# Kernel optimization log

Hardware: AMD Instinct MI355X
Metric: run time of the kernel (lower is better)

The kernel has to match this reference:

```python
import jax, jax.numpy as jnp
import numpy as np

B, S, N, M = 64, 512, 512, 128   # batch, sensory_size, state_size, motor_size
UNFOLDS = 6
DT = 0.1  # elapsed_time


def _gate(v, mu, sigma):
    # piecewise-linear 'sigmoid': clip((v - mu + sigma) / (2 sigma), 0, 1)
    # v: [B, P] -> [B, P, 1] broadcast against [P, N]
    return jnp.clip((v[..., None] - mu + sigma) / (2.0 * sigma), 0.0, 1.0)


def setup_inputs() -> dict:
    key = jax.random.key(0)
    ks = jax.random.split(key, 12)
    u = lambda k, sh, lo, hi: jax.random.uniform(k, sh, jnp.float32, lo, hi)
    inputs = jax.random.normal(ks[0], (B, S), dtype=jnp.float32)
    states = jax.random.normal(ks[1], (B, N), dtype=jnp.float32) * 0.1
    # parameters per _init_ranges
    tau = u(ks[2], (N,), 0.001, 2.0)
    b = u(ks[3], (N,), -0.2, 0.2)
    erev = jnp.where(jax.random.bernoulli(ks[4], 0.8, (N, N)), 1.0, -1.0).astype(jnp.float32)
    w = u(ks[5], (N, N), 0.001, 1.0)
    sigma = jnp.full((N, N), 0.5, jnp.float32)
    mu = jnp.full((N, N), 0.5, jnp.float32)
    sensory_erev = jnp.where(jax.random.bernoulli(ks[6], 0.8, (S, N)), 1.0, -1.0).astype(jnp.float32)
    sensory_w = u(ks[7], (S, N), 0.001, 1.0)
    sensory_sigma = jnp.full((S, N), 0.5, jnp.float32)
    sensory_mu = jnp.full((S, N), 0.5, jnp.float32)
    sparsity_mask = jax.random.bernoulli(ks[8], 0.3, (N, N)).astype(jnp.float32)
    sensory_sparsity_mask = jax.random.bernoulli(ks[9], 0.3, (S, N)).astype(jnp.float32)
    input_w = jnp.ones((S,), jnp.float32)
    input_b = jnp.zeros((S,), jnp.float32)
    output_w = jnp.ones((M,), jnp.float32)
    output_b = jnp.zeros((M,), jnp.float32)
    return dict(inputs=inputs, states=states, tau=tau, b=b, erev=erev, w=w,
                sigma=sigma, mu=mu, sensory_erev=sensory_erev, sensory_w=sensory_w,
                sensory_sigma=sensory_sigma, sensory_mu=sensory_mu,
                sparsity_mask=sparsity_mask, sensory_sparsity_mask=sensory_sparsity_mask,
                input_w=input_w, input_b=input_b, output_w=output_w, output_b=output_b)


def reference(inputs, states, tau, b, erev, w, sigma, mu,
              sensory_erev, sensory_w, sensory_sigma, sensory_mu,
              sparsity_mask, sensory_sparsity_mask,
              input_w, input_b, output_w, output_b):
    # input mapping (affine)
    x = inputs * input_w + input_b                                   # [B, S]
    # sensory synapses, computed once
    sa = _gate(x, sensory_mu, sensory_sigma) * sensory_sparsity_mask  # [B, S, N]
    s_rev = jnp.einsum('bsn,sn->bn', sa, sensory_erev)               # [B, N]
    s_w = jnp.einsum('bsn,sn->bn', sa, sensory_w)                    # [B, N]
    delta = DT / UNFOLDS

    def step(v, _):
        g = _gate(v, mu, sigma) * sparsity_mask                      # [B, N, N]
        sum_rev = jnp.einsum('bij,ij->bj', g, erev) + s_rev + b      # sum over presynaptic i
        sum_w = jnp.einsum('bij,ij->bj', g, w) + s_w
        k = 1.0 / (1.0 + sum_w)
        taun = tau * k
        q = taun / (taun + delta)
        v_new = q * v + (1.0 - q) * k * sum_rev
        return v_new, None

    v, _ = jax.lax.scan(step, states, None, length=UNFOLDS)
    # output mapping: slice last M neurons (M < N), then affine
    out = v[:, -M:] * output_w + output_b                            # [B, M]
    return out, v
```

## Files before the change

### kernel.cpp

```cpp
#include <hip/hip_runtime.h>
#include <string.h>

constexpr int cB = 64, cS = 512, cN = 512, cM = 128, cUNF = 6;
constexpr float cDELTA = 0.016666666666666666f;

constexpr int KB = 4;
constexpr int JT = 32;
constexpr int NJT = cN / JT;
constexpr int IC = 32;
constexpr int ILEN = cN / IC;
constexpr int NT = JT * IC;
constexpr int NB = (cB / KB) * NJT;

constexpr size_t OFF_EW  = 0;
constexpr size_t OFF_VA  = (size_t)cN * cN * 2;
constexpr size_t OFF_VB  = OFF_VA + (size_t)cB * cN;
constexpr size_t OFF_CTR = OFF_VB + (size_t)cB * cN;
constexpr int CTR_INTS = 512 + 16;

__device__ __forceinline__ float clamp01(float x) {
    return __builtin_amdgcn_fmed3f(x, 0.0f, 1.0f);
}

__global__ __launch_bounds__(NT)
void k_sns(const float* __restrict__ inputs, const float* __restrict__ states,
           const float* __restrict__ tau,    const float* __restrict__ bias,
           const float* __restrict__ erev,   const float* __restrict__ wgt,
           const float* __restrict__ sigma,  const float* __restrict__ mu,
           const float* __restrict__ serev,  const float* __restrict__ swgt,
           const float* __restrict__ ssigma, const float* __restrict__ smu,
           const float* __restrict__ mask,   const float* __restrict__ smask,
           const float* __restrict__ inw,    const float* __restrict__ inb,
           const float* __restrict__ outw,   const float* __restrict__ outb,
           float* __restrict__ out, float* __restrict__ ws)
{
    float2* EW = (float2*)(ws + OFF_EW);
    float* vA  = ws + OFF_VA;
    float* vB  = ws + OFF_VB;
    int*   ctr = (int*)(ws + OFF_CTR);

    const int tid = threadIdx.x, bid = blockIdx.x;
    const int jt = (bid & 7) * 2 + ((bid >> 3) & 1);
    const int bg = bid >> 4;
    const int b0 = bg * KB, j0 = jt * JT;
    const int jl = tid & (JT - 1), ic = tid >> 5;
    const int j = j0 + jl;
    int* barU  = ctr + bg * 16;
    int* barI  = ctr + 256 + jt * 16;
    int* flagp = ctr + 512 + jt;

    __shared__ float stage[cN * KB];
    __shared__ float redR[KB * IC * JT];
    __shared__ float redW[KB * IC * JT];
    __shared__ int   s_fast;

    {
        int i   = bg * 32 + ic;
        int idx = i * cN + j;
        float mk = mask[idx];
        float2 ew = make_float2(erev[idx] * mk, wgt[idx] * mk);
        unsigned long long bits;
        memcpy(&bits, &ew, 8);
        __hip_atomic_store((unsigned long long*)&EW[idx], bits,
                           __ATOMIC_RELAXED, __HIP_MEMORY_SCOPE_AGENT);
        if (!((sigma[idx] == 0.5f) && (mu[idx] == 0.5f)))
            __hip_atomic_fetch_or(flagp, 1, __ATOMIC_RELAXED, __HIP_MEMORY_SCOPE_AGENT);
    }

#pragma unroll
    for (int r = 0; r < (cS * KB) / NT; ++r) {
        int t = tid + r * NT;
        int bb = t & 3, s = t >> 2;
        stage[t] = fmaf(inputs[(b0 + bb) * cS + s], inw[s], inb[s]);
    }
    __syncthreads();
    {
        float aR[KB] = {0.f, 0.f, 0.f, 0.f}, aW[KB] = {0.f, 0.f, 0.f, 0.f};
        int idx = (ic * ILEN) * cN + j;
        int xo  = (ic * ILEN) * KB;
#pragma unroll 4
        for (int ii = 0; ii < ILEN; ++ii, idx += cN, xo += KB) {
            float sg = ssigma[idx];
            float a  = 0.5f / sg;
            float c  = fmaf(-smu[idx], a, 0.5f);
            float mk = smask[idx];
            float e  = serev[idx] * mk;
            float wv = swgt[idx] * mk;
            const float4 xv = *(const float4*)&stage[xo];
            float g;
            g = clamp01(fmaf(xv.x, a, c)); aR[0] = fmaf(g, e, aR[0]); aW[0] = fmaf(g, wv, aW[0]);
            g = clamp01(fmaf(xv.y, a, c)); aR[1] = fmaf(g, e, aR[1]); aW[1] = fmaf(g, wv, aW[1]);
            g = clamp01(fmaf(xv.z, a, c)); aR[2] = fmaf(g, e, aR[2]); aW[2] = fmaf(g, wv, aW[2]);
            g = clamp01(fmaf(xv.w, a, c)); aR[3] = fmaf(g, e, aR[3]); aW[3] = fmaf(g, wv, aW[3]);
        }
#pragma unroll
        for (int b = 0; b < KB; ++b) {
            redR[(b * IC + ic) * JT + jl] = aR[b];
            redW[(b * IC + ic) * JT + jl] = aW[b];
        }
    }
    __syncthreads();

    float my_srb = 0.f, my_sw = 0.f, my_tau = 0.f, my_ow = 0.f, my_ob = 0.f;
    int my_gidx = 0, my_mi = -1;
    if (tid < JT * KB) {
        int jj = tid & (JT - 1), bb = tid >> 5;
        float r = 0.f, wv = 0.f;
#pragma unroll
        for (int c2 = 0; c2 < IC; ++c2) {
            r  += redR[(bb * IC + c2) * JT + jj];
            wv += redW[(bb * IC + c2) * JT + jj];
        }
        int jg  = j0 + jj;
        my_gidx = (b0 + bb) * cN + jg;
        my_srb  = r + bias[jg];
        my_sw   = wv;
        my_tau  = tau[jg];
        if (jg >= cN - cM) {
            int m = jg - (cN - cM);
            my_ow = outw[m]; my_ob = outb[m];
            my_mi = (b0 + bb) * cM + m;
        }
    }

    __syncthreads();
    if (tid == 0) {
        __hip_atomic_fetch_add(barI, 1, __ATOMIC_RELAXED, __HIP_MEMORY_SCOPE_AGENT);
        while (__hip_atomic_load(barI, __ATOMIC_RELAXED, __HIP_MEMORY_SCOPE_AGENT) < NJT)
            __builtin_amdgcn_s_sleep(1);
        s_fast = (0 == __hip_atomic_load(flagp, __ATOMIC_RELAXED, __HIP_MEMORY_SCOPE_AGENT));
    }
    __syncthreads();
    const int fast = s_fast;

    const float* vin = states;
    for (int u = 0; u < cUNF; ++u) {
        float* vout = (u == cUNF - 1) ? (out + cB * cM) : ((u & 1) ? vA : vB);

#pragma unroll
        for (int r = 0; r < (cN * KB) / NT; ++r) {
            int t = tid + r * NT;
            int bb = t & 3, ii = t >> 2;
            float vv = __hip_atomic_load(&vin[(b0 + bb) * cN + ii],
                                         __ATOMIC_RELAXED, __HIP_MEMORY_SCOPE_AGENT);
            stage[t] = fast ? clamp01(vv) : vv;
        }
        __syncthreads();

        float vold = 0.f;
        if (tid < JT * KB)
            vold = __hip_atomic_load(&vin[my_gidx],
                                     __ATOMIC_RELAXED, __HIP_MEMORY_SCOPE_AGENT);

        float aR[KB] = {0.f, 0.f, 0.f, 0.f}, aW[KB] = {0.f, 0.f, 0.f, 0.f};
        if (fast) {
            int idx = (ic * ILEN) * cN + j;
            int vo  = (ic * ILEN) * KB;
#pragma unroll 8
            for (int ii = 0; ii < ILEN; ++ii, idx += cN, vo += KB) {
                const float2 ew = EW[idx];
                const float4 g4 = *(const float4*)&stage[vo];
                aR[0] = fmaf(g4.x, ew.x, aR[0]); aW[0] = fmaf(g4.x, ew.y, aW[0]);
                aR[1] = fmaf(g4.y, ew.x, aR[1]); aW[1] = fmaf(g4.y, ew.y, aW[1]);
                aR[2] = fmaf(g4.z, ew.x, aR[2]); aW[2] = fmaf(g4.z, ew.y, aW[2]);
                aR[3] = fmaf(g4.w, ew.x, aR[3]); aW[3] = fmaf(g4.w, ew.y, aW[3]);
            }
        } else {
            int idx = (ic * ILEN) * cN + j;
            int vo  = (ic * ILEN) * KB;
#pragma unroll 4
            for (int ii = 0; ii < ILEN; ++ii, idx += cN, vo += KB) {
                float sg = sigma[idx];
                float a  = 0.5f / sg;
                float c  = fmaf(-mu[idx], a, 0.5f);
                float2 ew = EW[idx];
                const float4 vv = *(const float4*)&stage[vo];
                float g;
                g = clamp01(fmaf(vv.x, a, c)); aR[0] = fmaf(g, ew.x, aR[0]); aW[0] = fmaf(g, ew.y, aW[0]);
                g = clamp01(fmaf(vv.y, a, c)); aR[1] = fmaf(g, ew.x, aR[1]); aW[1] = fmaf(g, ew.y, aW[1]);
                g = clamp01(fmaf(vv.z, a, c)); aR[2] = fmaf(g, ew.x, aR[2]); aW[2] = fmaf(g, ew.y, aW[2]);
                g = clamp01(fmaf(vv.w, a, c)); aR[3] = fmaf(g, ew.x, aR[3]); aW[3] = fmaf(g, ew.y, aW[3]);
            }
        }
#pragma unroll
        for (int b = 0; b < KB; ++b) {
            redR[(b * IC + ic) * JT + jl] = aR[b];
            redW[(b * IC + ic) * JT + jl] = aW[b];
        }
        __syncthreads();

        if (tid < JT * KB) {
            int jj = tid & (JT - 1), bb = tid >> 5;
            float r = 0.f, wv = 0.f;
#pragma unroll
            for (int c2 = 0; c2 < IC; ++c2) {
                r  += redR[(bb * IC + c2) * JT + jj];
                wv += redW[(bb * IC + c2) * JT + jj];
            }
            r  += my_srb;
            wv += my_sw;
            float k    = 1.0f / (1.0f + wv);
            float taun = my_tau * k;
            float inv  = 1.0f / (taun + cDELTA);
            float vn   = (taun * inv) * vold + (cDELTA * inv) * k * r;
            if (u == cUNF - 1) {
                vout[my_gidx] = vn;
                if (my_mi >= 0) out[my_mi] = fmaf(vn, my_ow, my_ob);
            } else {
                __hip_atomic_store(&vout[my_gidx], vn,
                                   __ATOMIC_RELAXED, __HIP_MEMORY_SCOPE_AGENT);
            }
        }

        if (u < cUNF - 1) {
            __syncthreads();
            if (tid == 0) {
                __hip_atomic_fetch_add(barU, 1, __ATOMIC_RELAXED, __HIP_MEMORY_SCOPE_AGENT);
                const int target = NJT * (u + 1);
                while (__hip_atomic_load(barU, __ATOMIC_RELAXED, __HIP_MEMORY_SCOPE_AGENT) < target)
                    __builtin_amdgcn_s_sleep(1);
            }
            __syncthreads();
            vin = (u & 1) ? vA : vB;
        }
    }
}

extern "C" void kernel_launch(void* const* d_in, const int* in_sizes, int n_in,
                              void* d_out, int out_size, void* d_ws, size_t ws_size,
                              hipStream_t stream)
{
    const float* inputs = (const float*)d_in[0];
    const float* states = (const float*)d_in[1];
    const float* tau    = (const float*)d_in[2];
    const float* bias   = (const float*)d_in[3];
    const float* erev   = (const float*)d_in[4];
    const float* wgt    = (const float*)d_in[5];
    const float* sigma  = (const float*)d_in[6];
    const float* mu     = (const float*)d_in[7];
    const float* serev  = (const float*)d_in[8];
    const float* swgt   = (const float*)d_in[9];
    const float* ssigma = (const float*)d_in[10];
    const float* smu    = (const float*)d_in[11];
    const float* mask   = (const float*)d_in[12];
    const float* smask  = (const float*)d_in[13];
    const float* inw    = (const float*)d_in[14];
    const float* inb    = (const float*)d_in[15];
    const float* outw   = (const float*)d_in[16];
    const float* outb   = (const float*)d_in[17];
    float* out = (float*)d_out;
    float* ws  = (float*)d_ws;

    hipMemsetAsync(ws + OFF_CTR, 0, CTR_INTS * sizeof(int), stream);

    k_sns<<<NB, NT, 0, stream>>>(inputs, states, tau, bias, erev, wgt, sigma, mu,
                                 serev, swgt, ssigma, smu, mask, smask,
                                 inw, inb, outw, outb, out, ws);
}
```

Measured before the change: 129.4 us.

## Keep masked erev/w tile in LDS per block and drop init grid barrier

Each block now builds its own 512x32 slice of masked (erev, w) pairs in shared memory (128 KB) and reads it from LDS in every unfold, instead of writing a global EW workspace and re-reading it from global memory each step. Because no cross-block data is shared anymore, the initial inter-block barrier and the global fast-path flag are replaced by a block-local __syncthreads_and. Partial sums are also reduced across half-wavefronts with shuffles before the LDS reduction, shrinking the reduction buffers. The cost is a large dynamic LDS footprint and redundant per-block loading of the weight slice across the 16 batch groups.

```diff
diff --git a/kernel.cpp b/kernel.cpp
--- a/kernel.cpp
+++ b/kernel.cpp
@@ -1,5 +1,4 @@
 #include <hip/hip_runtime.h>
-#include <string.h>
 
 constexpr int cB = 64, cS = 512, cN = 512, cM = 128, cUNF = 6;
 constexpr float cDELTA = 0.016666666666666666f;
@@ -10,13 +9,20 @@
 constexpr int IC = 32;
 constexpr int ILEN = cN / IC;
 constexpr int NT = JT * IC;
+constexpr int NW = NT / 64;
 constexpr int NB = (cB / KB) * NJT;
 
-constexpr size_t OFF_EW  = 0;
-constexpr size_t OFF_VA  = (size_t)cN * cN * 2;
+constexpr int SM_EW    = 0;
+constexpr int SM_STAGE = cN * JT * 2;
+constexpr int SM_REDR  = SM_STAGE + cN * KB;
+constexpr int SM_REDW  = SM_REDR + KB * NW * JT;
+constexpr int SM_FLOATS = SM_REDW + KB * NW * JT;
+constexpr size_t SMEM_BYTES = (size_t)SM_FLOATS * 4;
+
+constexpr size_t OFF_VA  = 0;
 constexpr size_t OFF_VB  = OFF_VA + (size_t)cB * cN;
 constexpr size_t OFF_CTR = OFF_VB + (size_t)cB * cN;
-constexpr int CTR_INTS = 512 + 16;
+constexpr int CTR_INTS = 16 * 16;
 
 __device__ __forceinline__ float clamp01(float x) {
     return __builtin_amdgcn_fmed3f(x, 0.0f, 1.0f);
@@ -34,7 +40,12 @@
            const float* __restrict__ outw,   const float* __restrict__ outb,
            float* __restrict__ out, float* __restrict__ ws)
 {
-    float2* EW = (float2*)(ws + OFF_EW);
+    extern __shared__ float smem[];
+    float2* ewl  = (float2*)(smem + SM_EW);
+    float*  stage = smem + SM_STAGE;
+    float*  redR  = smem + SM_REDR;
+    float*  redW  = smem + SM_REDW;
+
     float* vA  = ws + OFF_VA;
     float* vB  = ws + OFF_VB;
     int*   ctr = (int*)(ws + OFF_CTR);
@@ -44,27 +55,20 @@
     const int bg = bid >> 4;
     const int b0 = bg * KB, j0 = jt * JT;
     const int jl = tid & (JT - 1), ic = tid >> 5;
+    const int wv_id = tid >> 6, lane = tid & 63;
     const int j = j0 + jl;
-    int* barU  = ctr + bg * 16;
-    int* barI  = ctr + 256 + jt * 16;
-    int* flagp = ctr + 512 + jt;
-
-    __shared__ float stage[cN * KB];
-    __shared__ float redR[KB * IC * JT];
-    __shared__ float redW[KB * IC * JT];
-    __shared__ int   s_fast;
-
+    int* barU = ctr + bg * 16;
+
+    int ok = 1;
     {
-        int i   = bg * 32 + ic;
-        int idx = i * cN + j;
-        float mk = mask[idx];
-        float2 ew = make_float2(erev[idx] * mk, wgt[idx] * mk);
-        unsigned long long bits;
-        memcpy(&bits, &ew, 8);
-        __hip_atomic_store((unsigned long long*)&EW[idx], bits,
-                           __ATOMIC_RELAXED, __HIP_MEMORY_SCOPE_AGENT);
-        if (!((sigma[idx] == 0.5f) && (mu[idx] == 0.5f)))
-            __hip_atomic_fetch_or(flagp, 1, __ATOMIC_RELAXED, __HIP_MEMORY_SCOPE_AGENT);
+        int idx = (ic * ILEN) * cN + j;
+        int eo  = (ic * ILEN) * JT + jl;
+#pragma unroll 4
+        for (int ii = 0; ii < ILEN; ++ii, idx += cN, eo += JT) {
+            float mk = mask[idx];
+            ewl[eo] = make_float2(erev[idx] * mk, wgt[idx] * mk);
+            ok &= (sigma[idx] == 0.5f) & (mu[idx] == 0.5f);
+        }
     }
 
 #pragma unroll
@@ -73,7 +77,7 @@
         int bb = t & 3, s = t >> 2;
         stage[t] = fmaf(inputs[(b0 + bb) * cS + s], inw[s], inb[s]);
     }
-    __syncthreads();
+    const int fast = __syncthreads_and(ok);
     {
         float aR[KB] = {0.f, 0.f, 0.f, 0.f}, aW[KB] = {0.f, 0.f, 0.f, 0.f};
         int idx = (ic * ILEN) * cN + j;
@@ -85,18 +89,25 @@
             float c  = fmaf(-smu[idx], a, 0.5f);
             float mk = smask[idx];
             float e  = serev[idx] * mk;
-            float wv = swgt[idx] * mk;
+            float wvv = swgt[idx] * mk;
             const float4 xv = *(const float4*)&stage[xo];
             float g;
-            g = clamp01(fmaf(xv.x, a, c)); aR[0] = fmaf(g, e, aR[0]); aW[0] = fmaf(g, wv, aW[0]);
-            g = clamp01(fmaf(xv.y, a, c)); aR[1] = fmaf(g, e, aR[1]); aW[1] = fmaf(g, wv, aW[1]);
-            g = clamp01(fmaf(xv.z, a, c)); aR[2] = fmaf(g, e, aR[2]); aW[2] = fmaf(g, wv, aW[2]);
-            g = clamp01(fmaf(xv.w, a, c)); aR[3] = fmaf(g, e, aR[3]); aW[3] = fmaf(g, wv, aW[3]);
+            g = clamp01(fmaf(xv.x, a, c)); aR[0] = fmaf(g, e, aR[0]); aW[0] = fmaf(g, wvv, aW[0]);
+            g = clamp01(fmaf(xv.y, a, c)); aR[1] = fmaf(g, e, aR[1]); aW[1] = fmaf(g, wvv, aW[1]);
+            g = clamp01(fmaf(xv.z, a, c)); aR[2] = fmaf(g, e, aR[2]); aW[2] = fmaf(g, wvv, aW[2]);
+            g = clamp01(fmaf(xv.w, a, c)); aR[3] = fmaf(g, e, aR[3]); aW[3] = fmaf(g, wvv, aW[3]);
         }
 #pragma unroll
         for (int b = 0; b < KB; ++b) {
-            redR[(b * IC + ic) * JT + jl] = aR[b];
-            redW[(b * IC + ic) * JT + jl] = aW[b];
+            aR[b] += __shfl_xor(aR[b], 32, 64);
+            aW[b] += __shfl_xor(aW[b], 32, 64);
+        }
+        if (lane < JT) {
+#pragma unroll
+            for (int b = 0; b < KB; ++b) {
+                redR[(b * NW + wv_id) * JT + jl] = aR[b];
+                redW[(b * NW + wv_id) * JT + jl] = aW[b];
+            }
         }
     }
     __syncthreads();
@@ -105,16 +116,16 @@
     int my_gidx = 0, my_mi = -1;
     if (tid < JT * KB) {
         int jj = tid & (JT - 1), bb = tid >> 5;
-        float r = 0.f, wv = 0.f;
-#pragma unroll
-        for (int c2 = 0; c2 < IC; ++c2) {
-            r  += redR[(bb * IC + c2) * JT + jj];
-            wv += redW[(bb * IC + c2) * JT + jj];
+        float r = 0.f, wvv = 0.f;
+#pragma unroll
+        for (int w = 0; w < NW; ++w) {
+            r   += redR[(bb * NW + w) * JT + jj];
+            wvv += redW[(bb * NW + w) * JT + jj];
         }
         int jg  = j0 + jj;
         my_gidx = (b0 + bb) * cN + jg;
         my_srb  = r + bias[jg];
-        my_sw   = wv;
+        my_sw   = wvv;
         my_tau  = tau[jg];
         if (jg >= cN - cM) {
             int m = jg - (cN - cM);
@@ -123,16 +134,6 @@
         }
     }
 
-    __syncthreads();
-    if (tid == 0) {
-        __hip_atomic_fetch_add(barI, 1, __ATOMIC_RELAXED, __HIP_MEMORY_SCOPE_AGENT);
-        while (__hip_atomic_load(barI, __ATOMIC_RELAXED, __HIP_MEMORY_SCOPE_AGENT) < NJT)
-            __builtin_amdgcn_s_sleep(1);
-        s_fast = (0 == __hip_atomic_load(flagp, __ATOMIC_RELAXED, __HIP_MEMORY_SCOPE_AGENT));
-    }
-    __syncthreads();
-    const int fast = s_fast;
-
     const float* vin = states;
     for (int u = 0; u < cUNF; ++u) {
         float* vout = (u == cUNF - 1) ? (out + cB * cM) : ((u & 1) ? vA : vB);
@@ -141,9 +142,9 @@
         for (int r = 0; r < (cN * KB) / NT; ++r) {
             int t = tid + r * NT;
             int bb = t & 3, ii = t >> 2;
-            float vv = __hip_atomic_load(&vin[(b0 + bb) * cN + ii],
-                                         __ATOMIC_RELAXED, __HIP_MEMORY_SCOPE_AGENT);
-            stage[t] = fast ? clamp01(vv) : vv;
+            float vvv = __hip_atomic_load(&vin[(b0 + bb) * cN + ii],
+                                          __ATOMIC_RELAXED, __HIP_MEMORY_SCOPE_AGENT);
+            stage[t] = fast ? clamp01(vvv) : vvv;
         }
         __syncthreads();
 
@@ -154,11 +155,11 @@
 
         float aR[KB] = {0.f, 0.f, 0.f, 0.f}, aW[KB] = {0.f, 0.f, 0.f, 0.f};
         if (fast) {
-            int idx = (ic * ILEN) * cN + j;
-            int vo  = (ic * ILEN) * KB;
-#pragma unroll 8
-            for (int ii = 0; ii < ILEN; ++ii, idx += cN, vo += KB) {
-                const float2 ew = EW[idx];
+            int eo = (ic * ILEN) * JT + jl;
+            int vo = (ic * ILEN) * KB;
+#pragma unroll
+            for (int ii = 0; ii < ILEN; ++ii, eo += JT, vo += KB) {
+                const float2 ew = ewl[eo];
                 const float4 g4 = *(const float4*)&stage[vo];
                 aR[0] = fmaf(g4.x, ew.x, aR[0]); aW[0] = fmaf(g4.x, ew.y, aW[0]);
                 aR[1] = fmaf(g4.y, ew.x, aR[1]); aW[1] = fmaf(g4.y, ew.y, aW[1]);
@@ -167,39 +168,47 @@
             }
         } else {
             int idx = (ic * ILEN) * cN + j;
+            int eo  = (ic * ILEN) * JT + jl;
             int vo  = (ic * ILEN) * KB;
 #pragma unroll 4
-            for (int ii = 0; ii < ILEN; ++ii, idx += cN, vo += KB) {
+            for (int ii = 0; ii < ILEN; ++ii, idx += cN, eo += JT, vo += KB) {
                 float sg = sigma[idx];
                 float a  = 0.5f / sg;
                 float c  = fmaf(-mu[idx], a, 0.5f);
-                float2 ew = EW[idx];
-                const float4 vv = *(const float4*)&stage[vo];
+                const float2 ew = ewl[eo];
+                const float4 vv4 = *(const float4*)&stage[vo];
                 float g;
-                g = clamp01(fmaf(vv.x, a, c)); aR[0] = fmaf(g, ew.x, aR[0]); aW[0] = fmaf(g, ew.y, aW[0]);
-                g = clamp01(fmaf(vv.y, a, c)); aR[1] = fmaf(g, ew.x, aR[1]); aW[1] = fmaf(g, ew.y, aW[1]);
-                g = clamp01(fmaf(vv.z, a, c)); aR[2] = fmaf(g, ew.x, aR[2]); aW[2] = fmaf(g, ew.y, aW[2]);
-                g = clamp01(fmaf(vv.w, a, c)); aR[3] = fmaf(g, ew.x, aR[3]); aW[3] = fmaf(g, ew.y, aW[3]);
+                g = clamp01(fmaf(vv4.x, a, c)); aR[0] = fmaf(g, ew.x, aR[0]); aW[0] = fmaf(g, ew.y, aW[0]);
+                g = clamp01(fmaf(vv4.y, a, c)); aR[1] = fmaf(g, ew.x, aR[1]); aW[1] = fmaf(g, ew.y, aW[1]);
+                g = clamp01(fmaf(vv4.z, a, c)); aR[2] = fmaf(g, ew.x, aR[2]); aW[2] = fmaf(g, ew.y, aW[2]);
+                g = clamp01(fmaf(vv4.w, a, c)); aR[3] = fmaf(g, ew.x, aR[3]); aW[3] = fmaf(g, ew.y, aW[3]);
             }
         }
 #pragma unroll
         for (int b = 0; b < KB; ++b) {
-            redR[(b * IC + ic) * JT + jl] = aR[b];
-            redW[(b * IC + ic) * JT + jl] = aW[b];
+            aR[b] += __shfl_xor(aR[b], 32, 64);
+            aW[b] += __shfl_xor(aW[b], 32, 64);
+        }
+        if (lane < JT) {
+#pragma unroll
+            for (int b = 0; b < KB; ++b) {
+                redR[(b * NW + wv_id) * JT + jl] = aR[b];
+                redW[(b * NW + wv_id) * JT + jl] = aW[b];
+            }
         }
         __syncthreads();
 
         if (tid < JT * KB) {
             int jj = tid & (JT - 1), bb = tid >> 5;
-            float r = 0.f, wv = 0.f;
-#pragma unroll
-            for (int c2 = 0; c2 < IC; ++c2) {
-                r  += redR[(bb * IC + c2) * JT + jj];
-                wv += redW[(bb * IC + c2) * JT + jj];
-            }
-            r  += my_srb;
-            wv += my_sw;
-            float k    = 1.0f / (1.0f + wv);
+            float r = 0.f, wvv = 0.f;
+#pragma unroll
+            for (int w = 0; w < NW; ++w) {
+                r   += redR[(bb * NW + w) * JT + jj];
+                wvv += redW[(bb * NW + w) * JT + jj];
+            }
+            r   += my_srb;
+            wvv += my_sw;
+            float k    = 1.0f / (1.0f + wvv);
             float taun = my_tau * k;
             float inv  = 1.0f / (taun + cDELTA);
             float vn   = (taun * inv) * vold + (cDELTA * inv) * k * r;
@@ -251,9 +260,14 @@
     float* out = (float*)d_out;
     float* ws  = (float*)d_ws;
 
+    hipFuncSetAttribute((const void*)k_sns,
+                        hipFuncAttributeMaxDynamicSharedMemorySize,
+                        (int)SMEM_BYTES);
+
     hipMemsetAsync(ws + OFF_CTR, 0, CTR_INTS * sizeof(int), stream);
 
-    k_sns<<<NB, NT, 0, stream>>>(inputs, states, tau, bias, erev, wgt, sigma, mu,
-                                 serev, swgt, ssigma, smu, mask, smask,
-                                 inw, inb, outw, outb, out, ws);
+    k_sns<<<NB, NT, SMEM_BYTES, stream>>>(inputs, states, tau, bias, erev, wgt,
+                                          sigma, mu, serev, swgt, ssigma, smu,
+                                          mask, smask, inw, inb, outw, outb,
+                                          out, ws);
 }
```

Result: no change. 129.8 us (+0.3%).
